# Performance work log

Measured on AMD Instinct MI355X. Metric: run time of the kernel, lower is better.

The kernel has to match this reference:

```python
import jax, jax.numpy as jnp
import numpy as np

N = 50000      # num nodes
E = 600000     # num edges (avg degree 12)
IN = 256       # in_feats
H = 128        # h_feats
P = 2          # prop_step
LN_EPS = 1e-5


def setup_inputs() -> dict:
    key = jax.random.key(0)
    ks = jax.random.split(key, 8)
    return {
        "in_feat": jax.random.normal(ks[0], (N, IN), jnp.float32),
        "row": jax.random.randint(ks[1], (E,), 0, N),  # target node of each edge
        "col": jax.random.randint(ks[2], (E,), 0, N),  # source node of each edge
        "lin_w": jax.random.normal(ks[3], (H, IN), jnp.float32) / np.sqrt(IN).astype(np.float32),
        "lin_b": jnp.zeros((H,), jnp.float32),
        "conv_w": jax.random.normal(ks[4], (H, H), jnp.float32) / np.sqrt(H).astype(np.float32),
        "conv_b": jnp.zeros((H,), jnp.float32),
        "root_emb": jax.random.normal(ks[5], (1, H), jnp.float32) * 0.02,
        "ln_gamma": jnp.ones((P, H), jnp.float32),
        "ln_beta": jnp.zeros((P, H), jnp.float32),
    }


def _layernorm(x, g, b):
    mu = jnp.mean(x, axis=-1, keepdims=True)
    var = jnp.mean(jnp.square(x - mu), axis=-1, keepdims=True)
    return (x - mu) * jax.lax.rsqrt(var + LN_EPS) * g + b


def reference(in_feat, row, col, lin_w, lin_b, conv_w, conv_b, root_emb, ln_gamma, ln_beta):
    n = in_feat.shape[0]
    h = in_feat @ lin_w.T + lin_b                      # [N, H]

    # OGB-style degree norm with +1 trick (original edges, row = target)
    deg = jax.ops.segment_sum(jnp.ones_like(row, dtype=h.dtype), row, num_segments=n) + 1.0
    deg_inv = 1.0 / deg                                # deg >= 1, never inf

    # GCNConv symmetric norm with self loops: D^-1/2 (A+I) D^-1/2
    loop = jnp.arange(n)
    r2 = jnp.concatenate([row, loop])                  # [E+N] targets
    c2 = jnp.concatenate([col, loop])                  # [E+N] sources
    d2 = jax.ops.segment_sum(jnp.ones_like(r2, dtype=h.dtype), r2, num_segments=n)
    dis = jnp.where(d2 > 0, jax.lax.rsqrt(jnp.maximum(d2, 1.0)), 0.0)
    ew = dis[r2] * dis[c2]                             # [E+N] edge weights

    root = root_emb[0]                                 # [H]
    ori = h
    for i in range(P):
        if i != 0:
            h = h + ori                                # residual
            h = _layernorm(h, ln_gamma[i], ln_beta[i])
            h = jax.nn.relu(h)
            # dropout=0.0 -> identity
        xw = h @ conv_w.T                              # [N, H]
        h_msg = jax.ops.segment_sum(ew[:, None] * xw[c2], r2, num_segments=n) + conv_b
        root_contrib = jax.nn.relu(h + root) * deg_inv[:, None]
        h = h_msg + root_contrib
    return h
```

## Files before the change

### kernel.cpp

```cpp
#include <hip/hip_runtime.h>

#define NN 50000
#define EE 600000
#define INF 256
#define HF 128
#define CEB ((EE + 255) / 256)

typedef __attribute__((ext_vector_type(8))) short short8;
typedef __attribute__((ext_vector_type(4))) float floatx4;

__device__ __forceinline__ unsigned short f32_to_bf16_rne(float x) {
    unsigned int u = __float_as_uint(x);
    unsigned int r = (u + 0x7FFFu + ((u >> 16) & 1u)) >> 16;
    return (unsigned short)r;
}
__device__ __forceinline__ float bf16_to_f32(unsigned short h) {
    return __uint_as_float(((unsigned int)h) << 16);
}
__device__ __forceinline__ float bf16lo_u32(unsigned int u) {
    return __uint_as_float(u << 16);
}
__device__ __forceinline__ float bf16hi_u32(unsigned int u) {
    return __uint_as_float(u & 0xFFFF0000u);
}
__device__ __forceinline__ void cvt_hilo8(float4 v0, float4 v1, short8& hs, short8& ls) {
    float x[8] = {v0.x, v0.y, v0.z, v0.w, v1.x, v1.y, v1.z, v1.w};
    union { short8 s; unsigned short u[8]; } H, L;
#pragma unroll
    for (int k = 0; k < 8; ++k) {
        unsigned short hi = f32_to_bf16_rne(x[k]);
        H.u[k] = hi;
        L.u[k] = f32_to_bf16_rne(x[k] - bf16_to_f32(hi));
    }
    hs = H.s;
    ls = L.s;
}

__global__ void count_and_prepack(const int* __restrict__ row, int* __restrict__ cnt,
                                  int* __restrict__ pos, int E,
                                  const float* __restrict__ lw, const float* __restrict__ cw,
                                  unsigned short* __restrict__ fl, unsigned short* __restrict__ fc) {
    int b = blockIdx.x;
    if (b < CEB) {
        int e = b * 256 + threadIdx.x;
        if (e < E) pos[e] = atomicAdd(&cnt[row[e]], 1);
        return;
    }
    int idx = (b - CEB) * 256 + threadIdx.x;
    const float* src;
    unsigned short* dst;
    int K, c;
    if (idx < 8192) {
        src = lw; dst = fl; K = INF; c = idx;
    } else if (idx < 12288) {
        src = cw; dst = fc; K = HF; c = idx - 8192;
    } else return;
    int lane = c & 63;
    int nt = (c >> 6) & 7;
    int hl = (c >> 9) & 1;
    int kc = c >> 10;
    int rw = nt * 16 + (lane & 15);
    int koff = kc * 32 + (lane >> 4) * 8;
    const float* p = &src[(size_t)rw * K + koff];
    float4 v0 = *reinterpret_cast<const float4*>(p);
    float4 v1 = *reinterpret_cast<const float4*>(p + 4);
    short8 hs, ls;
    cvt_hilo8(v0, v1, hs, ls);
    *reinterpret_cast<short8*>(&dst[(size_t)c * 8]) = hl ? ls : hs;
}

__global__ void scan_phase1(const int* __restrict__ cnt, int* __restrict__ bsum, int n) {
    __shared__ int sdata[256];
    int t = threadIdx.x;
    int i = blockIdx.x * 256 + t;
    sdata[t] = (i < n) ? cnt[i] : 0;
    __syncthreads();
    for (int s = 128; s > 0; s >>= 1) {
        if (t < s) sdata[t] += sdata[t + s];
        __syncthreads();
    }
    if (t == 0) bsum[blockIdx.x] = sdata[0];
}

__global__ void scan_phase3(const int* __restrict__ cnt, const int* __restrict__ bsum,
                            int* __restrict__ row_start,
                            float* __restrict__ deg_inv, float* __restrict__ dis,
                            int n, int nb, int E) {
    __shared__ int sb[256];
    __shared__ int sdata[256];
    int t = threadIdx.x;
    sb[t] = (t < nb) ? bsum[t] : 0;
    __syncthreads();
    for (int s = 1; s < 256; s <<= 1) {
        int add = (t >= s) ? sb[t - s] : 0;
        __syncthreads();
        sb[t] += add;
        __syncthreads();
    }
    int base = sb[blockIdx.x] - bsum[blockIdx.x];
    int i = blockIdx.x * 256 + t;
    int v = (i < n) ? cnt[i] : 0;
    sdata[t] = v;
    __syncthreads();
    for (int s = 1; s < 256; s <<= 1) {
        int add = (t >= s) ? sdata[t - s] : 0;
        __syncthreads();
        sdata[t] += add;
        __syncthreads();
    }
    if (i < n) {
        int ex = base + sdata[t] - v;
        row_start[i] = ex;
        float d = (float)(v + 1);
        deg_inv[i] = 1.0f / d;
        dis[i] = rsqrtf(d);
    }
    if (blockIdx.x == 0 && t == 0) row_start[n] = E;
}

__global__ void fill_csr(const int* __restrict__ row, const int* __restrict__ col,
                         const int* __restrict__ row_start, const int* __restrict__ pos,
                         int* __restrict__ csr_col, int E) {
    int e = blockIdx.x * blockDim.x + threadIdx.x;
    if (e < E) {
        int p = row_start[row[e]] + pos[e];
        __builtin_nontemporal_store(col[e], &csr_col[p]);
    }
}

template <int K, int MODE>
__global__ __launch_bounds__(256) void gemm_ldsw(
    const float* __restrict__ Af,
    const unsigned short* __restrict__ Ahg, const unsigned short* __restrict__ Alg,
    const unsigned short* __restrict__ Wf,
    const float* __restrict__ bias,
    float* __restrict__ C, unsigned short* __restrict__ Cbf,
    const float* __restrict__ h, const float* __restrict__ deg_inv,
    const float* __restrict__ dis, const float* __restrict__ root,
    const float* __restrict__ gamma, const float* __restrict__ beta,
    int M) {
    constexpr int NKC = K / 32;
    __shared__ unsigned short WS[2 * 8192];

    const int t = threadIdx.x;
    const int wave = t >> 6;
    const int lane = t & 63;
    const int lrow = lane & 15;
    const int quad = lane >> 4;
    const int bm = blockIdx.x * 64;
    int arow = bm + wave * 16 + lrow;
    if (arow >= M) arow = M - 1;

    floatx4 acc[8];
#pragma unroll
    for (int nt = 0; nt < 8; ++nt) acc[nt] = (floatx4){0.f, 0.f, 0.f, 0.f};

#pragma unroll
    for (int p = 0; p < NKC / 2; ++p) {
        if (p) __syncthreads();
        {
            const uint4* src = reinterpret_cast<const uint4*>(Wf + (size_t)p * 16384);
            uint4* dstl = reinterpret_cast<uint4*>(WS);
#pragma unroll
            for (int i = 0; i < 8; ++i) dstl[t + 256 * i] = src[t + 256 * i];
        }
        __syncthreads();
#pragma unroll
        for (int k2 = 0; k2 < 2; ++k2) {
            int kc = p * 2 + k2;
            short8 afh, afl;
            if (MODE == 0) {
                const float* ap = &Af[(size_t)arow * K + kc * 32 + quad * 8];
                float4 a0 = *reinterpret_cast<const float4*>(ap);
                float4 a1 = *reinterpret_cast<const float4*>(ap + 4);
                cvt_hilo8(a0, a1, afh, afl);
            } else {
                size_t ao = (size_t)arow * K + kc * 32 + quad * 8;
                afh = *reinterpret_cast<const short8*>(&Ahg[ao]);
                afl = *reinterpret_cast<const short8*>(&Alg[ao]);
            }
            const unsigned short* wb = &WS[k2 * 8192 + lane * 8];
#pragma unroll
            for (int nt = 0; nt < 8; ++nt) {
                short8 bfh = *reinterpret_cast<const short8*>(wb + nt * 512);
                short8 bfl = *reinterpret_cast<const short8*>(wb + 4096 + nt * 512);
                acc[nt] = __builtin_amdgcn_mfma_f32_16x16x32_bf16(afh, bfh, acc[nt], 0, 0, 0);
                acc[nt] = __builtin_amdgcn_mfma_f32_16x16x32_bf16(afl, bfh, acc[nt], 0, 0, 0);
                acc[nt] = __builtin_amdgcn_mfma_f32_16x16x32_bf16(afh, bfl, acc[nt], 0, 0, 0);
            }
        }
    }

    float cb[8], rt[8], gm[8], bt[8];
#pragma unroll
    for (int nt = 0; nt < 8; ++nt) {
        int colh = nt * 16 + lrow;
        cb[nt] = bias[colh];
        if (MODE >= 1) rt[nt] = root[colh];
        if (MODE == 1) { gm[nt] = gamma[colh]; bt[nt] = beta[colh]; }
    }

#pragma unroll
    for (int r = 0; r < 4; ++r) {
        int grow = bm + wave * 16 + quad * 4 + r;
        bool ok = (grow < M);
        int gr = ok ? grow : M - 1;
        float x[8];
        if (MODE == 0) {
#pragma unroll
            for (int nt = 0; nt < 8; ++nt) x[nt] = acc[nt][r] + cb[nt];
        } else {
            float di = deg_inv[gr];
            float hv[8];
#pragma unroll
            for (int nt = 0; nt < 8; ++nt) hv[nt] = h[(size_t)gr * HF + nt * 16 + lrow];
#pragma unroll
            for (int nt = 0; nt < 8; ++nt) {
                float v = acc[nt][r] + cb[nt] + fmaxf(hv[nt] + rt[nt], 0.f) * di;
                x[nt] = (MODE == 1) ? v + hv[nt] : v;
            }
        }
        if (MODE == 1) {
            float s = 0.f;
#pragma unroll
            for (int nt = 0; nt < 8; ++nt) s += x[nt];
#pragma unroll
            for (int m = 1; m < 16; m <<= 1) s += __shfl_xor(s, m, 64);
            float mu = s * (1.0f / HF);
            float var = 0.f;
#pragma unroll
            for (int nt = 0; nt < 8; ++nt) { float d = x[nt] - mu; var += d * d; }
#pragma unroll
            for (int m = 1; m < 16; m <<= 1) var += __shfl_xor(var, m, 64);
            float rs = rsqrtf(var * (1.0f / HF) + 1e-5f);
            float ds = dis[gr];
            if (ok) {
#pragma unroll
                for (int nt = 0; nt < 8; ++nt) {
                    int colh = nt * 16 + lrow;
                    float y = fmaxf((x[nt] - mu) * rs * gm[nt] + bt[nt], 0.f);
                    C[(size_t)grow * HF + colh] = y;
                    Cbf[(size_t)grow * HF + colh] = f32_to_bf16_rne(ds * y);
                }
            }
        } else if (MODE == 0) {
            if (ok) {
                float ds = dis[grow];
#pragma unroll
                for (int nt = 0; nt < 8; ++nt) {
                    int colh = nt * 16 + lrow;
                    C[(size_t)grow * HF + colh] = x[nt];
                    Cbf[(size_t)grow * HF + colh] = f32_to_bf16_rne(ds * x[nt]);
                }
            }
        } else {
            if (ok) {
#pragma unroll
                for (int nt = 0; nt < 8; ++nt)
                    C[(size_t)grow * HF + nt * 16 + lrow] = x[nt];
            }
        }
    }
}

__global__ void aggregate(const int* __restrict__ row_start, const int* __restrict__ csr_col,
                          const float* __restrict__ dis, const float* __restrict__ deg_inv,
                          const float* __restrict__ h, const unsigned short* __restrict__ hbf,
                          unsigned short* __restrict__ agg_hi, unsigned short* __restrict__ agg_lo,
                          int n) {
    int wid = (blockIdx.x * blockDim.x + threadIdx.x) >> 6;
    int lane = threadIdx.x & 63;
    if (wid >= n) return;
    int q = lane >> 4;
    int l16 = lane & 15;
    int s = row_start[wid];
    int e = row_start[wid + 1];
    float a0 = 0.f, a1 = 0.f, a2 = 0.f, a3 = 0.f, a4 = 0.f, a5 = 0.f, a6 = 0.f, a7 = 0.f;
    if (e - s <= 16) {
        int j0 = s + q;
        bool p0 = j0 < e, p1 = j0 + 4 < e, p2 = j0 + 8 < e, p3 = j0 + 12 < e;
        int c0 = p0 ? csr_col[j0] : 0;
        int c1 = p1 ? csr_col[j0 + 4] : 0;
        int c2 = p2 ? csr_col[j0 + 8] : 0;
        int c3 = p3 ? csr_col[j0 + 12] : 0;
        uint4 z = make_uint4(0, 0, 0, 0);
        uint4 g0 = z, g1 = z, g2 = z, g3 = z;
        if (p0) g0 = *reinterpret_cast<const uint4*>(&hbf[(size_t)c0 * HF + l16 * 8]);
        if (p1) g1 = *reinterpret_cast<const uint4*>(&hbf[(size_t)c1 * HF + l16 * 8]);
        if (p2) g2 = *reinterpret_cast<const uint4*>(&hbf[(size_t)c2 * HF + l16 * 8]);
        if (p3) g3 = *reinterpret_cast<const uint4*>(&hbf[(size_t)c3 * HF + l16 * 8]);
        a0 = bf16lo_u32(g0.x) + bf16lo_u32(g1.x) + bf16lo_u32(g2.x) + bf16lo_u32(g3.x);
        a1 = bf16hi_u32(g0.x) + bf16hi_u32(g1.x) + bf16hi_u32(g2.x) + bf16hi_u32(g3.x);
        a2 = bf16lo_u32(g0.y) + bf16lo_u32(g1.y) + bf16lo_u32(g2.y) + bf16lo_u32(g3.y);
        a3 = bf16hi_u32(g0.y) + bf16hi_u32(g1.y) + bf16hi_u32(g2.y) + bf16hi_u32(g3.y);
        a4 = bf16lo_u32(g0.z) + bf16lo_u32(g1.z) + bf16lo_u32(g2.z) + bf16lo_u32(g3.z);
        a5 = bf16hi_u32(g0.z) + bf16hi_u32(g1.z) + bf16hi_u32(g2.z) + bf16hi_u32(g3.z);
        a6 = bf16lo_u32(g0.w) + bf16lo_u32(g1.w) + bf16lo_u32(g2.w) + bf16lo_u32(g3.w);
        a7 = bf16hi_u32(g0.w) + bf16hi_u32(g1.w) + bf16hi_u32(g2.w) + bf16hi_u32(g3.w);
    } else {
        float b0 = 0.f, b1 = 0.f, b2 = 0.f, b3 = 0.f, b4 = 0.f, b5 = 0.f, b6 = 0.f, b7 = 0.f;
        int j = s + q;
        for (; j + 4 < e; j += 8) {
            int c0 = csr_col[j];
            int c1 = csr_col[j + 4];
            uint4 h0 = *reinterpret_cast<const uint4*>(&hbf[(size_t)c0 * HF + l16 * 8]);
            uint4 h1 = *reinterpret_cast<const uint4*>(&hbf[(size_t)c1 * HF + l16 * 8]);
            a0 += bf16lo_u32(h0.x); a1 += bf16hi_u32(h0.x);
            a2 += bf16lo_u32(h0.y); a3 += bf16hi_u32(h0.y);
            a4 += bf16lo_u32(h0.z); a5 += bf16hi_u32(h0.z);
            a6 += bf16lo_u32(h0.w); a7 += bf16hi_u32(h0.w);
            b0 += bf16lo_u32(h1.x); b1 += bf16hi_u32(h1.x);
            b2 += bf16lo_u32(h1.y); b3 += bf16hi_u32(h1.y);
            b4 += bf16lo_u32(h1.z); b5 += bf16hi_u32(h1.z);
            b6 += bf16lo_u32(h1.w); b7 += bf16hi_u32(h1.w);
        }
        if (j < e) {
            int c0 = csr_col[j];
            uint4 h0 = *reinterpret_cast<const uint4*>(&hbf[(size_t)c0 * HF + l16 * 8]);
            a0 += bf16lo_u32(h0.x); a1 += bf16hi_u32(h0.x);
            a2 += bf16lo_u32(h0.y); a3 += bf16hi_u32(h0.y);
            a4 += bf16lo_u32(h0.z); a5 += bf16hi_u32(h0.z);
            a6 += bf16lo_u32(h0.w); a7 += bf16hi_u32(h0.w);
        }
        a0 += b0; a1 += b1; a2 += b2; a3 += b3;
        a4 += b4; a5 += b5; a6 += b6; a7 += b7;
    }
#pragma unroll
    for (int m = 16; m < 64; m <<= 1) {
        a0 += __shfl_xor(a0, m, 64);
        a1 += __shfl_xor(a1, m, 64);
        a2 += __shfl_xor(a2, m, 64);
        a3 += __shfl_xor(a3, m, 64);
        a4 += __shfl_xor(a4, m, 64);
        a5 += __shfl_xor(a5, m, 64);
        a6 += __shfl_xor(a6, m, 64);
        a7 += __shfl_xor(a7, m, 64);
    }
    if (q == 0) {
        float dn = dis[wid];
        float di = deg_inv[wid];
        float4 hA = *reinterpret_cast<const float4*>(&h[(size_t)wid * HF + l16 * 8]);
        float4 hB = *reinterpret_cast<const float4*>(&h[(size_t)wid * HF + l16 * 8 + 4]);
        float o[8];
        o[0] = fmaf(dn, a0, di * hA.x);
        o[1] = fmaf(dn, a1, di * hA.y);
        o[2] = fmaf(dn, a2, di * hA.z);
        o[3] = fmaf(dn, a3, di * hA.w);
        o[4] = fmaf(dn, a4, di * hB.x);
        o[5] = fmaf(dn, a5, di * hB.y);
        o[6] = fmaf(dn, a6, di * hB.z);
        o[7] = fmaf(dn, a7, di * hB.w);
        unsigned short hi[8], lo[8];
#pragma unroll
        for (int k = 0; k < 8; ++k) {
            hi[k] = f32_to_bf16_rne(o[k]);
            lo[k] = f32_to_bf16_rne(o[k] - bf16_to_f32(hi[k]));
        }
        uint4 hp, lp;
        hp.x = (unsigned)hi[0] | ((unsigned)hi[1] << 16);
        hp.y = (unsigned)hi[2] | ((unsigned)hi[3] << 16);
        hp.z = (unsigned)hi[4] | ((unsigned)hi[5] << 16);
        hp.w = (unsigned)hi[6] | ((unsigned)hi[7] << 16);
        lp.x = (unsigned)lo[0] | ((unsigned)lo[1] << 16);
        lp.y = (unsigned)lo[2] | ((unsigned)lo[3] << 16);
        lp.z = (unsigned)lo[4] | ((unsigned)lo[5] << 16);
        lp.w = (unsigned)lo[6] | ((unsigned)lo[7] << 16);
        *reinterpret_cast<uint4*>(&agg_hi[(size_t)wid * HF + l16 * 8]) = hp;
        *reinterpret_cast<uint4*>(&agg_lo[(size_t)wid * HF + l16 * 8]) = lp;
    }
}

extern "C" void kernel_launch(void* const* d_in, const int* in_sizes, int n_in,
                              void* d_out, int out_size, void* d_ws, size_t ws_size,
                              hipStream_t stream) {
    const int N = NN, E = EE;
    const float* in_feat = (const float*)d_in[0];
    const int* row = (const int*)d_in[1];
    const int* col = (const int*)d_in[2];
    const float* lin_w = (const float*)d_in[3];
    const float* lin_b = (const float*)d_in[4];
    const float* conv_w = (const float*)d_in[5];
    const float* conv_b = (const float*)d_in[6];
    const float* root_emb = (const float*)d_in[7];
    const float* ln_gamma = (const float*)d_in[8];
    const float* ln_beta = (const float*)d_in[9];
    float* out = (float*)d_out;

    float* ws = (float*)d_ws;
    size_t o = 0;
    float* deg_inv = ws + o; o += N;
    float* dis = ws + o; o += N;
    int* cnt = (int*)(ws + o); o += N;
    int* row_start = (int*)(ws + o); o += N + 4;
    int* pos = (int*)(ws + o); o += E;
    int* bsum = (int*)(ws + o); o += 256;
    int* csr_col = (int*)(ws + o); o += E;
    o = (o + 3) & ~(size_t)3;
    unsigned short* fl = (unsigned short*)(ws + o); o += 32768;
    unsigned short* fc = (unsigned short*)(ws + o); o += 16384;
    float* h0 = ws + o; o += (size_t)N * HF;
    unsigned short* hbf = (unsigned short*)(ws + o); o += (size_t)N * HF / 2;
    unsigned short* agg_hi = (unsigned short*)(ws + o); o += (size_t)N * HF / 2;
    unsigned short* agg_lo = (unsigned short*)(ws + o); o += (size_t)N * HF / 2;

    const int NB = (N + 255) / 256;

    hipMemsetAsync(cnt, 0, N * sizeof(int), stream);
    count_and_prepack<<<CEB + 48, 256, 0, stream>>>(row, cnt, pos, E, lin_w, conv_w, fl, fc);
    scan_phase1<<<NB, 256, 0, stream>>>(cnt, bsum, N);
    scan_phase3<<<NB, 256, 0, stream>>>(cnt, bsum, row_start, deg_inv, dis, N, NB, E);
    fill_csr<<<CEB, 256, 0, stream>>>(row, col, row_start, pos, csr_col, E);

    const int GB = (N + 63) / 64;
    const int WB = (N + 3) / 4;

    gemm_ldsw<INF, 0><<<GB, 256, 0, stream>>>(in_feat, nullptr, nullptr, fl, lin_b,
                                              h0, hbf, nullptr, nullptr, dis, nullptr,
                                              nullptr, nullptr, N);

    aggregate<<<WB, 256, 0, stream>>>(row_start, csr_col, dis, deg_inv, h0, hbf,
                                      agg_hi, agg_lo, N);
    gemm_ldsw<HF, 1><<<GB, 256, 0, stream>>>(nullptr, agg_hi, agg_lo, fc, conv_b,
                                             h0, hbf, h0, deg_inv, dis, root_emb,
                                             ln_gamma + HF, ln_beta + HF, N);

    aggregate<<<WB, 256, 0, stream>>>(row_start, csr_col, dis, deg_inv, h0, hbf,
                                      agg_hi, agg_lo, N);
    gemm_ldsw<HF, 2><<<GB, 256, 0, stream>>>(nullptr, agg_hi, agg_lo, fc, conv_b,
                                             out, nullptr, h0, deg_inv, dis, root_emb,
                                             nullptr, nullptr, N);
}
```

Measured before the change: 290.3 us.

## Fuse all stages into one cooperative persistent kernel with grid syncs

Replaces the sequence of separate launches (memset, count, scans, CSR fill, three GEMMs, two aggregations) with a single cooperative persistent kernel that uses grid-wide syncs between phases and grid-stride loops over tiles and nodes. It also overlaps the CSR fill with the first GEMM, since neither depends on the other. The goal is to remove launch gaps and tail effects between the many small kernels. The cost is a capped grid of up to 5 blocks per CU, which limits occupancy for the memory-bound aggregation, plus the overhead of each grid sync. A multi-kernel fallback path is kept.

```diff
diff --git a/kernel.cpp b/kernel.cpp
--- a/kernel.cpp
+++ b/kernel.cpp
@@ -1,10 +1,15 @@
 #include <hip/hip_runtime.h>
+#include <hip/hip_cooperative_groups.h>
+
+namespace cg = cooperative_groups;
 
 #define NN 50000
 #define EE 600000
 #define INF 256
 #define HF 128
 #define CEB ((EE + 255) / 256)
+#define GB ((NN + 63) / 64)
+#define NBCH ((NN + 255) / 256)
 
 typedef __attribute__((ext_vector_type(8))) short short8;
 typedef __attribute__((ext_vector_type(4))) float floatx4;
@@ -36,25 +41,23 @@
     ls = L.s;
 }
 
-__global__ void count_and_prepack(const int* __restrict__ row, int* __restrict__ cnt,
-                                  int* __restrict__ pos, int E,
-                                  const float* __restrict__ lw, const float* __restrict__ cw,
-                                  unsigned short* __restrict__ fl, unsigned short* __restrict__ fc) {
-    int b = blockIdx.x;
-    if (b < CEB) {
-        int e = b * 256 + threadIdx.x;
-        if (e < E) pos[e] = atomicAdd(&cnt[row[e]], 1);
-        return;
-    }
-    int idx = (b - CEB) * 256 + threadIdx.x;
-    const float* src;
-    unsigned short* dst;
-    int K, c;
-    if (idx < 8192) {
-        src = lw; dst = fl; K = INF; c = idx;
-    } else if (idx < 12288) {
-        src = cw; dst = fc; K = HF; c = idx - 8192;
-    } else return;
+struct Args {
+    const float* in_feat; const int* row; const int* col;
+    const float* lin_w; const float* lin_b;
+    const float* conv_w; const float* conv_b;
+    const float* root_emb; const float* ln_gamma; const float* ln_beta;
+    float* out;
+    float* deg_inv; float* dis;
+    int* cnt; int* row_start; int* pos; int* bsum; int* csr_col;
+    unsigned short* fl; unsigned short* fc;
+    float* h0; unsigned short* hbf;
+    unsigned short* agg_hi; unsigned short* agg_lo;
+};
+
+__device__ __forceinline__ void prepack_one(const Args& a, int idx) {
+    const float* src; unsigned short* dst; int K, c;
+    if (idx < 8192) { src = a.lin_w; dst = a.fl; K = INF; c = idx; }
+    else            { src = a.conv_w; dst = a.fc; K = HF; c = idx - 8192; }
     int lane = c & 63;
     int nt = (c >> 6) & 7;
     int hl = (c >> 9) & 1;
@@ -69,220 +72,84 @@
     *reinterpret_cast<short8*>(&dst[(size_t)c * 8]) = hl ? ls : hs;
 }
 
-__global__ void scan_phase1(const int* __restrict__ cnt, int* __restrict__ bsum, int n) {
-    __shared__ int sdata[256];
+__device__ __forceinline__ void zero_prepack_body(const Args& a, int gtid, int T) {
+    for (int i = gtid; i < NN; i += T) a.cnt[i] = 0;
+    for (int i = gtid; i < 12288; i += T) prepack_one(a, i);
+}
+
+__device__ __forceinline__ void count_body(const Args& a, int gtid, int T) {
+    for (int e = gtid; e < EE; e += T) a.pos[e] = atomicAdd(&a.cnt[a.row[e]], 1);
+}
+
+__device__ __forceinline__ void scanA_body(const Args& a, int* sdata) {
     int t = threadIdx.x;
-    int i = blockIdx.x * 256 + t;
-    sdata[t] = (i < n) ? cnt[i] : 0;
-    __syncthreads();
-    for (int s = 128; s > 0; s >>= 1) {
-        if (t < s) sdata[t] += sdata[t + s];
-        __syncthreads();
-    }
-    if (t == 0) bsum[blockIdx.x] = sdata[0];
-}
-
-__global__ void scan_phase3(const int* __restrict__ cnt, const int* __restrict__ bsum,
-                            int* __restrict__ row_start,
-                            float* __restrict__ deg_inv, float* __restrict__ dis,
-                            int n, int nb, int E) {
-    __shared__ int sb[256];
-    __shared__ int sdata[256];
+    for (int c = blockIdx.x; c < NBCH; c += gridDim.x) {
+        int i = c * 256 + t;
+        sdata[t] = (i < NN) ? a.cnt[i] : 0;
+        __syncthreads();
+        for (int s = 128; s > 0; s >>= 1) {
+            if (t < s) sdata[t] += sdata[t + s];
+            __syncthreads();
+        }
+        if (t == 0) a.bsum[c] = sdata[0];
+        __syncthreads();
+    }
+}
+
+__device__ __forceinline__ void scanC_body(const Args& a, int* sb, int* sdata) {
     int t = threadIdx.x;
-    sb[t] = (t < nb) ? bsum[t] : 0;
-    __syncthreads();
-    for (int s = 1; s < 256; s <<= 1) {
-        int add = (t >= s) ? sb[t - s] : 0;
-        __syncthreads();
-        sb[t] += add;
-        __syncthreads();
-    }
-    int base = sb[blockIdx.x] - bsum[blockIdx.x];
-    int i = blockIdx.x * 256 + t;
-    int v = (i < n) ? cnt[i] : 0;
-    sdata[t] = v;
-    __syncthreads();
-    for (int s = 1; s < 256; s <<= 1) {
-        int add = (t >= s) ? sdata[t - s] : 0;
-        __syncthreads();
-        sdata[t] += add;
-        __syncthreads();
-    }
-    if (i < n) {
-        int ex = base + sdata[t] - v;
-        row_start[i] = ex;
-        float d = (float)(v + 1);
-        deg_inv[i] = 1.0f / d;
-        dis[i] = rsqrtf(d);
-    }
-    if (blockIdx.x == 0 && t == 0) row_start[n] = E;
-}
-
-__global__ void fill_csr(const int* __restrict__ row, const int* __restrict__ col,
-                         const int* __restrict__ row_start, const int* __restrict__ pos,
-                         int* __restrict__ csr_col, int E) {
-    int e = blockIdx.x * blockDim.x + threadIdx.x;
-    if (e < E) {
-        int p = row_start[row[e]] + pos[e];
-        __builtin_nontemporal_store(col[e], &csr_col[p]);
-    }
-}
-
-template <int K, int MODE>
-__global__ __launch_bounds__(256) void gemm_ldsw(
-    const float* __restrict__ Af,
-    const unsigned short* __restrict__ Ahg, const unsigned short* __restrict__ Alg,
-    const unsigned short* __restrict__ Wf,
-    const float* __restrict__ bias,
-    float* __restrict__ C, unsigned short* __restrict__ Cbf,
-    const float* __restrict__ h, const float* __restrict__ deg_inv,
-    const float* __restrict__ dis, const float* __restrict__ root,
-    const float* __restrict__ gamma, const float* __restrict__ beta,
-    int M) {
-    constexpr int NKC = K / 32;
-    __shared__ unsigned short WS[2 * 8192];
-
-    const int t = threadIdx.x;
-    const int wave = t >> 6;
-    const int lane = t & 63;
-    const int lrow = lane & 15;
-    const int quad = lane >> 4;
-    const int bm = blockIdx.x * 64;
-    int arow = bm + wave * 16 + lrow;
-    if (arow >= M) arow = M - 1;
-
-    floatx4 acc[8];
-#pragma unroll
-    for (int nt = 0; nt < 8; ++nt) acc[nt] = (floatx4){0.f, 0.f, 0.f, 0.f};
-
-#pragma unroll
-    for (int p = 0; p < NKC / 2; ++p) {
-        if (p) __syncthreads();
-        {
-            const uint4* src = reinterpret_cast<const uint4*>(Wf + (size_t)p * 16384);
-            uint4* dstl = reinterpret_cast<uint4*>(WS);
-#pragma unroll
-            for (int i = 0; i < 8; ++i) dstl[t + 256 * i] = src[t + 256 * i];
-        }
-        __syncthreads();
-#pragma unroll
-        for (int k2 = 0; k2 < 2; ++k2) {
-            int kc = p * 2 + k2;
-            short8 afh, afl;
-            if (MODE == 0) {
-                const float* ap = &Af[(size_t)arow * K + kc * 32 + quad * 8];
-                float4 a0 = *reinterpret_cast<const float4*>(ap);
-                float4 a1 = *reinterpret_cast<const float4*>(ap + 4);
-                cvt_hilo8(a0, a1, afh, afl);
-            } else {
-                size_t ao = (size_t)arow * K + kc * 32 + quad * 8;
-                afh = *reinterpret_cast<const short8*>(&Ahg[ao]);
-                afl = *reinterpret_cast<const short8*>(&Alg[ao]);
-            }
-            const unsigned short* wb = &WS[k2 * 8192 + lane * 8];
-#pragma unroll
-            for (int nt = 0; nt < 8; ++nt) {
-                short8 bfh = *reinterpret_cast<const short8*>(wb + nt * 512);
-                short8 bfl = *reinterpret_cast<const short8*>(wb + 4096 + nt * 512);
-                acc[nt] = __builtin_amdgcn_mfma_f32_16x16x32_bf16(afh, bfh, acc[nt], 0, 0, 0);
-                acc[nt] = __builtin_amdgcn_mfma_f32_16x16x32_bf16(afl, bfh, acc[nt], 0, 0, 0);
-                acc[nt] = __builtin_amdgcn_mfma_f32_16x16x32_bf16(afh, bfl, acc[nt], 0, 0, 0);
-            }
-        }
-    }
-
-    float cb[8], rt[8], gm[8], bt[8];
-#pragma unroll
-    for (int nt = 0; nt < 8; ++nt) {
-        int colh = nt * 16 + lrow;
-        cb[nt] = bias[colh];
-        if (MODE >= 1) rt[nt] = root[colh];
-        if (MODE == 1) { gm[nt] = gamma[colh]; bt[nt] = beta[colh]; }
-    }
-
-#pragma unroll
-    for (int r = 0; r < 4; ++r) {
-        int grow = bm + wave * 16 + quad * 4 + r;
-        bool ok = (grow < M);
-        int gr = ok ? grow : M - 1;
-        float x[8];
-        if (MODE == 0) {
-#pragma unroll
-            for (int nt = 0; nt < 8; ++nt) x[nt] = acc[nt][r] + cb[nt];
-        } else {
-            float di = deg_inv[gr];
-            float hv[8];
-#pragma unroll
-            for (int nt = 0; nt < 8; ++nt) hv[nt] = h[(size_t)gr * HF + nt * 16 + lrow];
-#pragma unroll
-            for (int nt = 0; nt < 8; ++nt) {
-                float v = acc[nt][r] + cb[nt] + fmaxf(hv[nt] + rt[nt], 0.f) * di;
-                x[nt] = (MODE == 1) ? v + hv[nt] : v;
-            }
-        }
-        if (MODE == 1) {
-            float s = 0.f;
-#pragma unroll
-            for (int nt = 0; nt < 8; ++nt) s += x[nt];
-#pragma unroll
-            for (int m = 1; m < 16; m <<= 1) s += __shfl_xor(s, m, 64);
-            float mu = s * (1.0f / HF);
-            float var = 0.f;
-#pragma unroll
-            for (int nt = 0; nt < 8; ++nt) { float d = x[nt] - mu; var += d * d; }
-#pragma unroll
-            for (int m = 1; m < 16; m <<= 1) var += __shfl_xor(var, m, 64);
-            float rs = rsqrtf(var * (1.0f / HF) + 1e-5f);
-            float ds = dis[gr];
-            if (ok) {
-#pragma unroll
-                for (int nt = 0; nt < 8; ++nt) {
-                    int colh = nt * 16 + lrow;
-                    float y = fmaxf((x[nt] - mu) * rs * gm[nt] + bt[nt], 0.f);
-                    C[(size_t)grow * HF + colh] = y;
-                    Cbf[(size_t)grow * HF + colh] = f32_to_bf16_rne(ds * y);
-                }
-            }
-        } else if (MODE == 0) {
-            if (ok) {
-                float ds = dis[grow];
-#pragma unroll
-                for (int nt = 0; nt < 8; ++nt) {
-                    int colh = nt * 16 + lrow;
-                    C[(size_t)grow * HF + colh] = x[nt];
-                    Cbf[(size_t)grow * HF + colh] = f32_to_bf16_rne(ds * x[nt]);
-                }
-            }
-        } else {
-            if (ok) {
-#pragma unroll
-                for (int nt = 0; nt < 8; ++nt)
-                    C[(size_t)grow * HF + nt * 16 + lrow] = x[nt];
-            }
-        }
-    }
-}
-
-__global__ void aggregate(const int* __restrict__ row_start, const int* __restrict__ csr_col,
-                          const float* __restrict__ dis, const float* __restrict__ deg_inv,
-                          const float* __restrict__ h, const unsigned short* __restrict__ hbf,
-                          unsigned short* __restrict__ agg_hi, unsigned short* __restrict__ agg_lo,
-                          int n) {
-    int wid = (blockIdx.x * blockDim.x + threadIdx.x) >> 6;
-    int lane = threadIdx.x & 63;
-    if (wid >= n) return;
+    for (int c = blockIdx.x; c < NBCH; c += gridDim.x) {
+        sb[t] = (t < NBCH) ? a.bsum[t] : 0;
+        __syncthreads();
+        for (int s = 1; s < 256; s <<= 1) {
+            int add = (t >= s) ? sb[t - s] : 0;
+            __syncthreads();
+            sb[t] += add;
+            __syncthreads();
+        }
+        int base = sb[c] - a.bsum[c];
+        int i = c * 256 + t;
+        int v = (i < NN) ? a.cnt[i] : 0;
+        sdata[t] = v;
+        __syncthreads();
+        for (int s = 1; s < 256; s <<= 1) {
+            int add = (t >= s) ? sdata[t - s] : 0;
+            __syncthreads();
+            sdata[t] += add;
+            __syncthreads();
+        }
+        if (i < NN) {
+            a.row_start[i] = base + sdata[t] - v;
+            float d = (float)(v + 1);
+            a.deg_inv[i] = 1.0f / d;
+            a.dis[i] = rsqrtf(d);
+        }
+        __syncthreads();
+    }
+    if (blockIdx.x == 0 && t == 0) a.row_start[NN] = EE;
+}
+
+__device__ __forceinline__ void fill_body(const Args& a, int gtid, int T) {
+    for (int e = gtid; e < EE; e += T) {
+        int pp = a.row_start[a.row[e]] + a.pos[e];
+        __builtin_nontemporal_store(a.col[e], &a.csr_col[pp]);
+    }
+}
+
+__device__ __forceinline__ void agg_node(const Args& p, int wid, int lane) {
     int q = lane >> 4;
     int l16 = lane & 15;
-    int s = row_start[wid];
-    int e = row_start[wid + 1];
+    int s = p.row_start[wid];
+    int e = p.row_start[wid + 1];
     float a0 = 0.f, a1 = 0.f, a2 = 0.f, a3 = 0.f, a4 = 0.f, a5 = 0.f, a6 = 0.f, a7 = 0.f;
+    const unsigned short* hbf = p.hbf;
     if (e - s <= 16) {
         int j0 = s + q;
         bool p0 = j0 < e, p1 = j0 + 4 < e, p2 = j0 + 8 < e, p3 = j0 + 12 < e;
-        int c0 = p0 ? csr_col[j0] : 0;
-        int c1 = p1 ? csr_col[j0 + 4] : 0;
-        int c2 = p2 ? csr_col[j0 + 8] : 0;
-        int c3 = p3 ? csr_col[j0 + 12] : 0;
+        int c0 = p0 ? p.csr_col[j0] : 0;
+        int c1 = p1 ? p.csr_col[j0 + 4] : 0;
+        int c2 = p2 ? p.csr_col[j0 + 8] : 0;
+        int c3 = p3 ? p.csr_col[j0 + 12] : 0;
         uint4 z = make_uint4(0, 0, 0, 0);
         uint4 g0 = z, g1 = z, g2 = z, g3 = z;
         if (p0) g0 = *reinterpret_cast<const uint4*>(&hbf[(size_t)c0 * HF + l16 * 8]);
@@ -301,8 +168,8 @@
         float b0 = 0.f, b1 = 0.f, b2 = 0.f, b3 = 0.f, b4 = 0.f, b5 = 0.f, b6 = 0.f, b7 = 0.f;
         int j = s + q;
         for (; j + 4 < e; j += 8) {
-            int c0 = csr_col[j];
-            int c1 = csr_col[j + 4];
+            int c0 = p.csr_col[j];
+            int c1 = p.csr_col[j + 4];
             uint4 h0 = *reinterpret_cast<const uint4*>(&hbf[(size_t)c0 * HF + l16 * 8]);
             uint4 h1 = *reinterpret_cast<const uint4*>(&hbf[(size_t)c1 * HF + l16 * 8]);
             a0 += bf16lo_u32(h0.x); a1 += bf16hi_u32(h0.x);
@@ -315,7 +182,7 @@
             b6 += bf16lo_u32(h1.w); b7 += bf16hi_u32(h1.w);
         }
         if (j < e) {
-            int c0 = csr_col[j];
+            int c0 = p.csr_col[j];
             uint4 h0 = *reinterpret_cast<const uint4*>(&hbf[(size_t)c0 * HF + l16 * 8]);
             a0 += bf16lo_u32(h0.x); a1 += bf16hi_u32(h0.x);
             a2 += bf16lo_u32(h0.y); a3 += bf16hi_u32(h0.y);
@@ -337,10 +204,10 @@
         a7 += __shfl_xor(a7, m, 64);
     }
     if (q == 0) {
-        float dn = dis[wid];
-        float di = deg_inv[wid];
-        float4 hA = *reinterpret_cast<const float4*>(&h[(size_t)wid * HF + l16 * 8]);
-        float4 hB = *reinterpret_cast<const float4*>(&h[(size_t)wid * HF + l16 * 8 + 4]);
+        float dn = p.dis[wid];
+        float di = p.deg_inv[wid];
+        float4 hA = *reinterpret_cast<const float4*>(&p.h0[(size_t)wid * HF + l16 * 8]);
+        float4 hB = *reinterpret_cast<const float4*>(&p.h0[(size_t)wid * HF + l16 * 8 + 4]);
         float o[8];
         o[0] = fmaf(dn, a0, di * hA.x);
         o[1] = fmaf(dn, a1, di * hA.y);
@@ -365,68 +232,259 @@
         lp.y = (unsigned)lo[2] | ((unsigned)lo[3] << 16);
         lp.z = (unsigned)lo[4] | ((unsigned)lo[5] << 16);
         lp.w = (unsigned)lo[6] | ((unsigned)lo[7] << 16);
-        *reinterpret_cast<uint4*>(&agg_hi[(size_t)wid * HF + l16 * 8]) = hp;
-        *reinterpret_cast<uint4*>(&agg_lo[(size_t)wid * HF + l16 * 8]) = lp;
-    }
+        *reinterpret_cast<uint4*>(&p.agg_hi[(size_t)wid * HF + l16 * 8]) = hp;
+        *reinterpret_cast<uint4*>(&p.agg_lo[(size_t)wid * HF + l16 * 8]) = lp;
+    }
+}
+
+template <int K, int MODE>
+__device__ __forceinline__ void gemm_tile(const Args& p, int bidx, unsigned short* WS) {
+    constexpr int NKC = K / 32;
+    const int t = threadIdx.x;
+    const int wave = t >> 6;
+    const int lane = t & 63;
+    const int lrow = lane & 15;
+    const int quad = lane >> 4;
+    const int bm = bidx * 64;
+    int arow = bm + wave * 16 + lrow;
+    if (arow >= NN) arow = NN - 1;
+
+    const unsigned short* Wf = (MODE == 0) ? p.fl : p.fc;
+
+    floatx4 acc[8];
+#pragma unroll
+    for (int nt = 0; nt < 8; ++nt) acc[nt] = (floatx4){0.f, 0.f, 0.f, 0.f};
+
+#pragma unroll
+    for (int pp = 0; pp < NKC / 2; ++pp) {
+        __syncthreads();
+        {
+            const uint4* src = reinterpret_cast<const uint4*>(Wf + (size_t)pp * 16384);
+            uint4* dstl = reinterpret_cast<uint4*>(WS);
+#pragma unroll
+            for (int i = 0; i < 8; ++i) dstl[t + 256 * i] = src[t + 256 * i];
+        }
+        __syncthreads();
+#pragma unroll
+        for (int k2 = 0; k2 < 2; ++k2) {
+            int kc = pp * 2 + k2;
+            short8 afh, afl;
+            if (MODE == 0) {
+                const float* ap = &p.in_feat[(size_t)arow * K + kc * 32 + quad * 8];
+                float4 a0 = *reinterpret_cast<const float4*>(ap);
+                float4 a1 = *reinterpret_cast<const float4*>(ap + 4);
+                cvt_hilo8(a0, a1, afh, afl);
+            } else {
+                size_t ao = (size_t)arow * K + kc * 32 + quad * 8;
+                afh = *reinterpret_cast<const short8*>(&p.agg_hi[ao]);
+                afl = *reinterpret_cast<const short8*>(&p.agg_lo[ao]);
+            }
+            const unsigned short* wb = &WS[k2 * 8192 + lane * 8];
+#pragma unroll
+            for (int nt = 0; nt < 8; ++nt) {
+                short8 bfh = *reinterpret_cast<const short8*>(wb + nt * 512);
+                short8 bfl = *reinterpret_cast<const short8*>(wb + 4096 + nt * 512);
+                acc[nt] = __builtin_amdgcn_mfma_f32_16x16x32_bf16(afh, bfh, acc[nt], 0, 0, 0);
+                acc[nt] = __builtin_amdgcn_mfma_f32_16x16x32_bf16(afl, bfh, acc[nt], 0, 0, 0);
+                acc[nt] = __builtin_amdgcn_mfma_f32_16x16x32_bf16(afh, bfl, acc[nt], 0, 0, 0);
+            }
+        }
+    }
+
+    const float* bias = (MODE == 0) ? p.lin_b : p.conv_b;
+    float* C = (MODE == 2) ? p.out : p.h0;
+
+    float cb[8], rt[8], gm[8], bt[8];
+#pragma unroll
+    for (int nt = 0; nt < 8; ++nt) {
+        int colh = nt * 16 + lrow;
+        cb[nt] = bias[colh];
+        if (MODE >= 1) rt[nt] = p.root_emb[colh];
+        if (MODE == 1) { gm[nt] = p.ln_gamma[HF + colh]; bt[nt] = p.ln_beta[HF + colh]; }
+    }
+
+#pragma unroll
+    for (int r = 0; r < 4; ++r) {
+        int grow = bm + wave * 16 + quad * 4 + r;
+        bool ok = (grow < NN);
+        int gr = ok ? grow : NN - 1;
+        float x[8];
+        if (MODE == 0) {
+#pragma unroll
+            for (int nt = 0; nt < 8; ++nt) x[nt] = acc[nt][r] + cb[nt];
+        } else {
+            float di = p.deg_inv[gr];
+            float hv[8];
+#pragma unroll
+            for (int nt = 0; nt < 8; ++nt) hv[nt] = p.h0[(size_t)gr * HF + nt * 16 + lrow];
+#pragma unroll
+            for (int nt = 0; nt < 8; ++nt) {
+                float v = acc[nt][r] + cb[nt] + fmaxf(hv[nt] + rt[nt], 0.f) * di;
+                x[nt] = (MODE == 1) ? v + hv[nt] : v;
+            }
+        }
+        if (MODE == 1) {
+            float s = 0.f;
+#pragma unroll
+            for (int nt = 0; nt < 8; ++nt) s += x[nt];
+#pragma unroll
+            for (int m = 1; m < 16; m <<= 1) s += __shfl_xor(s, m, 64);
+            float mu = s * (1.0f / HF);
+            float var = 0.f;
+#pragma unroll
+            for (int nt = 0; nt < 8; ++nt) { float d = x[nt] - mu; var += d * d; }
+#pragma unroll
+            for (int m = 1; m < 16; m <<= 1) var += __shfl_xor(var, m, 64);
+            float rs = rsqrtf(var * (1.0f / HF) + 1e-5f);
+            float ds = p.dis[gr];
+            if (ok) {
+#pragma unroll
+                for (int nt = 0; nt < 8; ++nt) {
+                    int colh = nt * 16 + lrow;
+                    float y = fmaxf((x[nt] - mu) * rs * gm[nt] + bt[nt], 0.f);
+                    C[(size_t)grow * HF + colh] = y;
+                    p.hbf[(size_t)grow * HF + colh] = f32_to_bf16_rne(ds * y);
+                }
+            }
+        } else if (MODE == 0) {
+            if (ok) {
+                float ds = p.dis[grow];
+#pragma unroll
+                for (int nt = 0; nt < 8; ++nt) {
+                    int colh = nt * 16 + lrow;
+                    C[(size_t)grow * HF + colh] = x[nt];
+                    p.hbf[(size_t)grow * HF + colh] = f32_to_bf16_rne(ds * x[nt]);
+                }
+            }
+        } else {
+            if (ok) {
+#pragma unroll
+                for (int nt = 0; nt < 8; ++nt)
+                    C[(size_t)grow * HF + nt * 16 + lrow] = x[nt];
+            }
+        }
+    }
+}
+
+__global__ __launch_bounds__(256) void mega(Args a) {
+    cg::grid_group grid = cg::this_grid();
+    extern __shared__ __align__(16) char smem[];
+    unsigned short* WS = reinterpret_cast<unsigned short*>(smem);
+    int* si = reinterpret_cast<int*>(smem);
+    const int T = gridDim.x * blockDim.x;
+    const int gtid = blockIdx.x * blockDim.x + threadIdx.x;
+    const int gwave = gtid >> 6;
+    const int nwave = T >> 6;
+    const int lane = threadIdx.x & 63;
+
+    zero_prepack_body(a, gtid, T);
+    grid.sync();
+    count_body(a, gtid, T);
+    grid.sync();
+    scanA_body(a, si);
+    grid.sync();
+    scanC_body(a, si, si + 256);
+    grid.sync();
+    fill_body(a, gtid, T);
+    for (int b = blockIdx.x; b < GB; b += gridDim.x) gemm_tile<INF, 0>(a, b, WS);
+    grid.sync();
+    for (int nd = gwave; nd < NN; nd += nwave) agg_node(a, nd, lane);
+    grid.sync();
+    for (int b = blockIdx.x; b < GB; b += gridDim.x) gemm_tile<HF, 1>(a, b, WS);
+    grid.sync();
+    for (int nd = gwave; nd < NN; nd += nwave) agg_node(a, nd, lane);
+    grid.sync();
+    for (int b = blockIdx.x; b < GB; b += gridDim.x) gemm_tile<HF, 2>(a, b, WS);
+}
+
+__global__ void k_pre(Args a)   { zero_prepack_body(a, blockIdx.x * blockDim.x + threadIdx.x, gridDim.x * blockDim.x); }
+__global__ void k_count(Args a) { count_body(a, blockIdx.x * blockDim.x + threadIdx.x, gridDim.x * blockDim.x); }
+__global__ void k_scanA(Args a) { extern __shared__ __align__(16) char s[]; scanA_body(a, (int*)s); }
+__global__ void k_scanC(Args a) { extern __shared__ __align__(16) char s[]; scanC_body(a, (int*)s, (int*)s + 256); }
+__global__ void k_fill(Args a)  { fill_body(a, blockIdx.x * blockDim.x + threadIdx.x, gridDim.x * blockDim.x); }
+__global__ void k_agg(Args a) {
+    int gw = (blockIdx.x * blockDim.x + threadIdx.x) >> 6;
+    int nw = (gridDim.x * blockDim.x) >> 6;
+    int lane = threadIdx.x & 63;
+    for (int nd = gw; nd < NN; nd += nw) agg_node(a, nd, lane);
+}
+template <int K, int MODE>
+__global__ __launch_bounds__(256) void k_gemm(Args a) {
+    extern __shared__ __align__(16) char s[];
+    unsigned short* WS = reinterpret_cast<unsigned short*>(s);
+    for (int b = blockIdx.x; b < GB; b += gridDim.x) gemm_tile<K, MODE>(a, b, WS);
 }
 
 extern "C" void kernel_launch(void* const* d_in, const int* in_sizes, int n_in,
                               void* d_out, int out_size, void* d_ws, size_t ws_size,
                               hipStream_t stream) {
     const int N = NN, E = EE;
-    const float* in_feat = (const float*)d_in[0];
-    const int* row = (const int*)d_in[1];
-    const int* col = (const int*)d_in[2];
-    const float* lin_w = (const float*)d_in[3];
-    const float* lin_b = (const float*)d_in[4];
-    const float* conv_w = (const float*)d_in[5];
-    const float* conv_b = (const float*)d_in[6];
-    const float* root_emb = (const float*)d_in[7];
-    const float* ln_gamma = (const float*)d_in[8];
-    const float* ln_beta = (const float*)d_in[9];
-    float* out = (float*)d_out;
+    Args a;
+    a.in_feat = (const float*)d_in[0];
+    a.row = (const int*)d_in[1];
+    a.col = (const int*)d_in[2];
+    a.lin_w = (const float*)d_in[3];
+    a.lin_b = (const float*)d_in[4];
+    a.conv_w = (const float*)d_in[5];
+    a.conv_b = (const float*)d_in[6];
+    a.root_emb = (const float*)d_in[7];
+    a.ln_gamma = (const float*)d_in[8];
+    a.ln_beta = (const float*)d_in[9];
+    a.out = (float*)d_out;
 
     float* ws = (float*)d_ws;
     size_t o = 0;
-    float* deg_inv = ws + o; o += N;
-    float* dis = ws + o; o += N;
-    int* cnt = (int*)(ws + o); o += N;
-    int* row_start = (int*)(ws + o); o += N + 4;
-    int* pos = (int*)(ws + o); o += E;
-    int* bsum = (int*)(ws + o); o += 256;
-    int* csr_col = (int*)(ws + o); o += E;
+    a.deg_inv = ws + o; o += N;
+    a.dis = ws + o; o += N;
+    a.cnt = (int*)(ws + o); o += N;
+    a.row_start = (int*)(ws + o); o += N + 4;
+    a.pos = (int*)(ws + o); o += E;
+    a.bsum = (int*)(ws + o); o += 256;
+    a.csr_col = (int*)(ws + o); o += E;
     o = (o + 3) & ~(size_t)3;
-    unsigned short* fl = (unsigned short*)(ws + o); o += 32768;
-    unsigned short* fc = (unsigned short*)(ws + o); o += 16384;
-    float* h0 = ws + o; o += (size_t)N * HF;
-    unsigned short* hbf = (unsigned short*)(ws + o); o += (size_t)N * HF / 2;
-    unsigned short* agg_hi = (unsigned short*)(ws + o); o += (size_t)N * HF / 2;
-    unsigned short* agg_lo = (unsigned short*)(ws + o); o += (size_t)N * HF / 2;
-
-    const int NB = (N + 255) / 256;
-
-    hipMemsetAsync(cnt, 0, N * sizeof(int), stream);
-    count_and_prepack<<<CEB + 48, 256, 0, stream>>>(row, cnt, pos, E, lin_w, conv_w, fl, fc);
-    scan_phase1<<<NB, 256, 0, stream>>>(cnt, bsum, N);
-    scan_phase3<<<NB, 256, 0, stream>>>(cnt, bsum, row_start, deg_inv, dis, N, NB, E);
-    fill_csr<<<CEB, 256, 0, stream>>>(row, col, row_start, pos, csr_col, E);
-
-    const int GB = (N + 63) / 64;
-    const int WB = (N + 3) / 4;
-
-    gemm_ldsw<INF, 0><<<GB, 256, 0, stream>>>(in_feat, nullptr, nullptr, fl, lin_b,
-                                              h0, hbf, nullptr, nullptr, dis, nullptr,
-                                              nullptr, nullptr, N);
-
-    aggregate<<<WB, 256, 0, stream>>>(row_start, csr_col, dis, deg_inv, h0, hbf,
-                                      agg_hi, agg_lo, N);
-    gemm_ldsw<HF, 1><<<GB, 256, 0, stream>>>(nullptr, agg_hi, agg_lo, fc, conv_b,
-                                             h0, hbf, h0, deg_inv, dis, root_emb,
-                                             ln_gamma + HF, ln_beta + HF, N);
-
-    aggregate<<<WB, 256, 0, stream>>>(row_start, csr_col, dis, deg_inv, h0, hbf,
-                                      agg_hi, agg_lo, N);
-    gemm_ldsw<HF, 2><<<GB, 256, 0, stream>>>(nullptr, agg_hi, agg_lo, fc, conv_b,
-                                             out, nullptr, h0, deg_inv, dis, root_emb,
-                                             nullptr, nullptr, N);
-}
+    a.fl = (unsigned short*)(ws + o); o += 32768;
+    a.fc = (unsigned short*)(ws + o); o += 16384;
+    a.h0 = ws + o; o += (size_t)N * HF;
+    a.hbf = (unsigned short*)(ws + o); o += (size_t)N * HF / 2;
+    a.agg_hi = (unsigned short*)(ws + o); o += (size_t)N * HF / 2;
+    a.agg_lo = (unsigned short*)(ws + o); o += (size_t)N * HF / 2;
+
+    constexpr unsigned int SHMEM = 32768;
+
+    static int nblk = 0;
+    static bool coop_ok = true;
+    if (nblk == 0) {
+        int dev = 0;
+        hipGetDevice(&dev);
+        int cus = 0;
+        hipError_t e0 = hipDeviceGetAttribute(&cus, hipDeviceAttributeMultiprocessorCount, dev);
+        int maxb = 0;
+        hipError_t e1 = hipOccupancyMaxActiveBlocksPerMultiprocessor(&maxb, mega, 256, (size_t)SHMEM);
+        if (e0 != hipSuccess || e1 != hipSuccess || cus < 1 || maxb < 1) {
+            coop_ok = false;
+            nblk = -1;
+        } else {
+            if (maxb > 5) maxb = 5;
+            nblk = cus * maxb;
+        }
+    }
+
+    if (coop_ok) {
+        void* args[] = { (void*)&a };
+        hipError_t err = hipLaunchCooperativeKernel(
+            reinterpret_cast<const void*>(&mega), dim3(nblk), dim3(256), args, SHMEM, stream);
+        if (err == hipSuccess) return;
+        coop_ok = false;
+    }
+
+    k_pre<<<256, 256, 0, stream>>>(a);
+    k_count<<<CEB, 256, 0, stream>>>(a);
+    k_scanA<<<NBCH, 256, 2048, stream>>>(a);
+    k_scanC<<<NBCH, 256, 2048, stream>>>(a);
+    k_fill<<<CEB, 256, 0, stream>>>(a);
+    k_gemm<INF, 0><<<GB, 256, SHMEM, stream>>>(a);
+    k_agg<<<(N + 3) / 4, 256, 0, stream>>>(a);
+    k_gemm<HF, 1><<<GB, 256, SHMEM, stream>>>(a);
+    k_agg<<<(N + 3) / 4, 256, 0, stream>>>(a);
+    k_gemm<HF, 2><<<GB, 256, SHMEM, stream>>>(a);
+}
```

Result: slower. 690.2 us (+137.8%).
